# Kernel tuning notes

Measured on AMD Instinct MI355X. Metric: run time of the kernel, lower is better.

## Reference

```python
import jax, jax.numpy as jnp
import numpy as np

B, T, C, HS = 8, 2048, 1024, 64


def setup_inputs() -> dict:
    key = jax.random.key(0)
    kx, kq, kk, kv = jax.random.split(key, 4)
    x = jax.random.normal(kx, (B, T, C), dtype=jnp.float32)
    # torch Linear(C, HS, bias=False): weight [HS, C], y = x @ W.T -> store as [C, HS]
    Wq = jax.random.normal(kq, (C, HS), dtype=jnp.float32) * (C ** -0.5)
    Wk = jax.random.normal(kk, (C, HS), dtype=jnp.float32) * (C ** -0.5)
    Wv = jax.random.normal(kv, (C, HS), dtype=jnp.float32) * (C ** -0.5)
    return {"x": x, "Wq": Wq, "Wk": Wk, "Wv": Wv}


def reference(x, Wq, Wk, Wv):
    _, t, c = x.shape
    q = jnp.einsum('btc,ch->bth', x, Wq)
    k = jnp.einsum('btc,ch->bth', x, Wk)
    v = jnp.einsum('btc,ch->bth', x, Wv)
    # NOTE: original scales by C**-0.5 (hidden_dim), not head_size**-0.5
    scores = jnp.einsum('bth,bsh->bts', q, k) * (c ** -0.5)  # [B,T,T]
    causal = jnp.tril(jnp.ones((t, t), dtype=bool))
    scores = jnp.where(causal, scores, -jnp.inf)
    probs = jax.nn.softmax(scores, axis=-1)  # dropout p=0.0 -> identity
    out = jnp.einsum('bts,bsh->bth', probs, v)  # [B,T,HS]
    return out
```

## Files before the change

### kernel.cpp

```cpp
#include <hip/hip_runtime.h>
#include <hip/hip_bf16.h>

#define B_ 8
#define T_ 2048
#define C_ 1024
#define HS_ 64

typedef float f32x4 __attribute__((ext_vector_type(4)));
typedef __bf16 bf16x8 __attribute__((ext_vector_type(8)));
typedef __bf16 bf16x4 __attribute__((ext_vector_type(4)));


__global__ __launch_bounds__(256) void wt_kernel(const float* __restrict__ Wq,
                                                 const float* __restrict__ Wk,
                                                 const float* __restrict__ Wv,
                                                 __bf16* __restrict__ wt) {
    __shared__ float tile[64][65];
    int mb = blockIdx.x >> 4;
    int k0 = (blockIdx.x & 15) * 64;
    const float* W = (mb == 0) ? Wq : (mb == 1 ? Wk : Wv);
    int c = threadIdx.x & 63;
#pragma unroll
    for (int r = threadIdx.x >> 6; r < 64; r += 4)
        tile[r][c] = W[(size_t)(k0 + r) * 64 + c];
    __syncthreads();
    float scale = (mb == 0) ? 0.03125f : 1.0f;
    int kk = threadIdx.x & 63;
#pragma unroll
    for (int n = threadIdx.x >> 6; n < 64; n += 4)
        wt[(size_t)(mb * 64 + n) * C_ + k0 + kk] = (__bf16)(tile[kk][n] * scale);
}

__global__ __launch_bounds__(512) void qkv_kernel(const float* __restrict__ x,
                                                  const __bf16* __restrict__ wt,
                                                  __bf16* __restrict__ qf,
                                                  __bf16* __restrict__ kf,
                                                  __bf16* __restrict__ vf) {
    __shared__ __align__(16) char smem[57344];
    __bf16* xs0 = (__bf16*)smem;
    __bf16* xs1 = (__bf16*)(smem + 4096);
    __bf16* ws0 = (__bf16*)(smem + 8192);
    __bf16* ws1 = (__bf16*)(smem + 32768);

    const int tid = threadIdx.x;
    const int w = tid >> 6, lane = tid & 63, lq = lane & 15, lg = lane >> 4;
    const int m0 = blockIdx.x * 32;
    const int mt = w & 1;
    const int ntb = (w >> 1) * 3;

    f32x4 acc[3];
#pragma unroll
    for (int i = 0; i < 3; ++i) acc[i] = (f32x4)0.0f;

    const int xrow = tid >> 3, xch = tid & 7;
    float4 xr0, xr1;
    bf16x8 wr[3];

    if (tid < 256) {
        const float* xp = x + (size_t)(m0 + xrow) * C_ + xch * 8;
        xr0 = *(const float4*)xp;
        xr1 = *(const float4*)(xp + 4);
    }
#pragma unroll
    for (int s = 0; s < 3; ++s) {
        int u = tid + s * 512;
        wr[s] = *(const bf16x8*)(wt + (size_t)(u >> 3) * C_ + (u & 7) * 8);
    }
    if (tid < 256) {
        bf16x8 xb;
#pragma unroll
        for (int j = 0; j < 4; ++j) { xb[j] = (__bf16)xr0[j]; xb[4 + j] = (__bf16)xr1[j]; }
        *(bf16x8*)(xs0 + xrow * 64 + ((xch ^ (xrow & 7)) * 8)) = xb;
    }
#pragma unroll
    for (int s = 0; s < 3; ++s) {
        int u = tid + s * 512, rw = u >> 3, ch = u & 7;
        *(bf16x8*)(ws0 + rw * 64 + ((ch ^ (rw & 7)) * 8)) = wr[s];
    }

    for (int kt = 0; kt < 16; ++kt) {
        __syncthreads();
        __bf16* xsc = (kt & 1) ? xs1 : xs0;
        __bf16* wsc = (kt & 1) ? ws1 : ws0;
        if (kt < 15) {
            int k0 = (kt + 1) * 64;
            if (tid < 256) {
                const float* xp = x + (size_t)(m0 + xrow) * C_ + k0 + xch * 8;
                xr0 = *(const float4*)xp;
                xr1 = *(const float4*)(xp + 4);
            }
#pragma unroll
            for (int s = 0; s < 3; ++s) {
                int u = tid + s * 512;
                wr[s] = *(const bf16x8*)(wt + (size_t)(u >> 3) * C_ + k0 + (u & 7) * 8);
            }
        }
#pragma unroll
        for (int ks = 0; ks < 2; ++ks) {
            int r = mt * 16 + lq;
            bf16x8 a = *(const bf16x8*)(xsc + r * 64 + (((ks * 4 + lg) ^ (r & 7)) * 8));
#pragma unroll
            for (int i = 0; i < 3; ++i) {
                int rw = (ntb + i) * 16 + lq;
                bf16x8 b = *(const bf16x8*)(wsc + rw * 64 + (((ks * 4 + lg) ^ (rw & 7)) * 8));
                acc[i] = __builtin_amdgcn_mfma_f32_16x16x32_bf16(a, b, acc[i], 0, 0, 0);
            }
        }
        if (kt < 15) {
            __bf16* xsn = (kt & 1) ? xs0 : xs1;
            __bf16* wsn = (kt & 1) ? ws0 : ws1;
            if (tid < 256) {
                bf16x8 xb;
#pragma unroll
                for (int j = 0; j < 4; ++j) { xb[j] = (__bf16)xr0[j]; xb[4 + j] = (__bf16)xr1[j]; }
                *(bf16x8*)(xsn + xrow * 64 + ((xch ^ (xrow & 7)) * 8)) = xb;
            }
#pragma unroll
            for (int s = 0; s < 3; ++s) {
                int u = tid + s * 512, rw = u >> 3, ch = u & 7;
                *(bf16x8*)(wsn + rw * 64 + ((ch ^ (rw & 7)) * 8)) = wr[s];
            }
        }
    }
    __syncthreads();

    __bf16(*obuf)[208] = (__bf16(*)[208])smem;
#pragma unroll
    for (int i = 0; i < 3; ++i)
#pragma unroll
        for (int r = 0; r < 4; ++r)
            obuf[mt * 16 + lg * 4 + r][(ntb + i) * 16 + lq] = (__bf16)acc[i][r];
    __syncthreads();

    if (w < 4) {
        int mg = w & 1, half = w >> 1;
        size_t qt16 = (size_t)(m0 >> 4) + mg;
        bf16x8 vq = *(const bf16x8*)&obuf[mg * 16 + lq][half * 32 + lg * 8];
        bf16x8 vk = *(const bf16x8*)&obuf[mg * 16 + lq][64 + half * 32 + lg * 8];
        *(bf16x8*)(qf + ((qt16 * 2 + half) * 64 + lane) * 8) = vq;
        *(bf16x8*)(kf + ((qt16 * 2 + half) * 64 + lane) * 8) = vk;
    } else {
        int ntv = w - 4;
        bf16x8 vv;
#pragma unroll
        for (int j = 0; j < 8; ++j)
            vv[j] = obuf[lg * 8 + j][128 + ntv * 16 + lq];
        size_t kt32 = (size_t)(m0 >> 5);
        *(bf16x8*)(vf + ((kt32 * 4 + ntv) * 64 + lane) * 8) = vv;
    }
}

__global__ __launch_bounds__(512) void attn_kernel(const __bf16* __restrict__ qf,
                                                   const __bf16* __restrict__ kf,
                                                   const __bf16* __restrict__ vf,
                                                   float* __restrict__ out) {
    __shared__ float olds[8][16][64];
    __shared__ float mlds[8][16], llds[8][16];
    __shared__ __align__(16) __bf16 plds[8][16 * 40];

    int w    = threadIdx.x >> 6;
    int lane = threadIdx.x & 63;
    int lq = lane & 15, lg = lane >> 4;

    int b  = blockIdx.x & 7;
    int t0 = (blockIdx.x >> 3) * 16;

    size_t qbase = ((size_t)b * 128 + (t0 >> 4)) * 2;
    bf16x8 aq0 = *(const bf16x8*)(qf + ((qbase + 0) * 64 + lane) * 8);
    bf16x8 aq1 = *(const bf16x8*)(qf + ((qbase + 1) * 64 + lane) * 8);

    f32x4 o[4];
#pragma unroll
    for (int nt = 0; nt < 4; ++nt) o[nt] = (f32x4)0.0f;
    float m_s = -1e30f, l_s = 0.f;

    __bf16* pw = &plds[w][0];

    int ntiles = (t0 + 47) >> 5;
    for (int kt = w; kt < ntiles; kt += 8) {
        int s0 = kt * 32;
        f32x4 s[2];
#pragma unroll
        for (int ct = 0; ct < 2; ++ct) {
            size_t kbase = ((size_t)b * 128 + (s0 >> 4) + ct) * 2;
            bf16x8 k0 = *(const bf16x8*)(kf + ((kbase + 0) * 64 + lane) * 8);
            bf16x8 k1 = *(const bf16x8*)(kf + ((kbase + 1) * 64 + lane) * 8);
            f32x4 a = (f32x4)0.0f;
            a = __builtin_amdgcn_mfma_f32_16x16x32_bf16(k0, aq0, a, 0, 0, 0);
            a = __builtin_amdgcn_mfma_f32_16x16x32_bf16(k1, aq1, a, 0, 0, 0);
            s[ct] = a;
        }
        if (s0 + 31 > t0) {
#pragma unroll
            for (int ct = 0; ct < 2; ++ct)
#pragma unroll
                for (int r = 0; r < 4; ++r)
                    if (s0 + ct * 16 + lg * 4 + r > t0 + lq) s[ct][r] = -1e30f;
        }
        float pm = fmaxf(fmaxf(fmaxf(s[0][0], s[0][1]), fmaxf(s[0][2], s[0][3])),
                         fmaxf(fmaxf(s[1][0], s[1][1]), fmaxf(s[1][2], s[1][3])));
        pm = fmaxf(pm, __shfl_xor(pm, 16));
        pm = fmaxf(pm, __shfl_xor(pm, 32));
        float mn = fmaxf(m_s, pm);
        float al = __expf(m_s - mn);
        m_s = mn;
        f32x4 p0, p1;
#pragma unroll
        for (int r = 0; r < 4; ++r) {
            p0[r] = __expf(s[0][r] - mn);
            p1[r] = __expf(s[1][r] - mn);
        }
        float rs = (p0[0] + p0[1]) + (p0[2] + p0[3]) +
                   (p1[0] + p1[1]) + (p1[2] + p1[3]);
        rs += __shfl_xor(rs, 16);
        rs += __shfl_xor(rs, 32);
        l_s = l_s * al + rs;
        float alr[4];
#pragma unroll
        for (int r = 0; r < 4; ++r) alr[r] = __shfl(al, lg * 4 + r);
#pragma unroll
        for (int nt = 0; nt < 4; ++nt)
#pragma unroll
            for (int r = 0; r < 4; ++r) o[nt][r] *= alr[r];

        bf16x4 q0, q1;
#pragma unroll
        for (int r = 0; r < 4; ++r) { q0[r] = (__bf16)p0[r]; q1[r] = (__bf16)p1[r]; }
        *(bf16x4*)&pw[lq * 40 + lg * 4]      = q0;
        *(bf16x4*)&pw[lq * 40 + 16 + lg * 4] = q1;
        asm volatile("" ::: "memory");
        bf16x8 pa = *(const bf16x8*)&pw[lq * 40 + lg * 8];
#pragma unroll
        for (int nt = 0; nt < 4; ++nt) {
            bf16x8 bv = *(const bf16x8*)(vf +
                (((size_t)(b * 64 + (s0 >> 5)) * 4 + nt) * 64 + lane) * 8);
            o[nt] = __builtin_amdgcn_mfma_f32_16x16x32_bf16(pa, bv, o[nt], 0, 0, 0);
        }
    }

    asm volatile("" ::: "memory");
#pragma unroll
    for (int nt = 0; nt < 4; ++nt)
#pragma unroll
        for (int r = 0; r < 4; ++r)
            olds[w][lg * 4 + r][nt * 16 + lq] = o[nt][r];
    if (lg == 0) {
        mlds[w][lq] = m_s;
        llds[w][lq] = l_s;
    }
    __syncthreads();

    int row = threadIdx.x >> 5;
    int col = (threadIdx.x & 31) * 2;
    float M = -1e30f;
#pragma unroll
    for (int w2 = 0; w2 < 8; ++w2) M = fmaxf(M, mlds[w2][row]);
    float L = 0.f, o0 = 0.f, o1 = 0.f;
#pragma unroll
    for (int w2 = 0; w2 < 8; ++w2) {
        float sc = __expf(mlds[w2][row] - M);
        L  += sc * llds[w2][row];
        o0 += sc * olds[w2][row][col];
        o1 += sc * olds[w2][row][col + 1];
    }
    float inv = 1.0f / L;
    float* ob = out + ((size_t)b * T_ + t0 + row) * HS_ + col;
    ob[0] = o0 * inv;
    ob[1] = o1 * inv;
}

extern "C" void kernel_launch(void* const* d_in, const int* in_sizes, int n_in,
                              void* d_out, int out_size, void* d_ws, size_t ws_size,
                              hipStream_t stream) {
    const float* x  = (const float*)d_in[0];
    const float* Wq = (const float*)d_in[1];
    const float* Wk = (const float*)d_in[2];
    const float* Wv = (const float*)d_in[3];
    char* ws = (char*)d_ws;
    __bf16* wt = (__bf16*)ws;
    __bf16* qf = (__bf16*)(ws + 393216);
    __bf16* kf = (__bf16*)(ws + 2490368);
    __bf16* vf = (__bf16*)(ws + 4587520);
    float* out = (float*)d_out;

    wt_kernel<<<dim3(48), dim3(256), 0, stream>>>(Wq, Wk, Wv, wt);
    qkv_kernel<<<dim3(512), dim3(512), 0, stream>>>(x, wt, qf, kf, vf);
    attn_kernel<<<dim3(1024), dim3(512), 0, stream>>>(qf, kf, vf, out);
}
```

Measured before the change: 41.06 us.

## Split QKV projection across N halves and enlarge attention query tiles

The QKV projection now launches twice as many 256-thread blocks, each computing half of the 192 output columns, so more blocks are resident and LDS use drops. The attention kernel now handles 32 query rows per block with 4 waves over 64-key tiles, reuses each K/V load across two query subtiles, orders blocks heaviest-first, and adds setprio around the MFMA sections. The output merge is vectorized to float4. These changes aim at better load balance and fewer global K/V loads per unit of work, at the cost of more registers per wave and fewer waves per block to split the key range.

```diff
diff --git a/kernel.cpp b/kernel.cpp
--- a/kernel.cpp
+++ b/kernel.cpp
@@ -31,20 +31,22 @@
         wt[(size_t)(mb * 64 + n) * C_ + k0 + kk] = (__bf16)(tile[kk][n] * scale);
 }
 
-__global__ __launch_bounds__(512) void qkv_kernel(const float* __restrict__ x,
-                                                  const __bf16* __restrict__ wt,
-                                                  __bf16* __restrict__ qf,
-                                                  __bf16* __restrict__ kf,
-                                                  __bf16* __restrict__ vf) {
-    __shared__ __align__(16) char smem[57344];
+__global__ __launch_bounds__(256, 4) void qkv_kernel(const float* __restrict__ x,
+                                                     const __bf16* __restrict__ wt,
+                                                     __bf16* __restrict__ qf,
+                                                     __bf16* __restrict__ kf,
+                                                     __bf16* __restrict__ vf) {
+    __shared__ __align__(16) char smem[32768];
     __bf16* xs0 = (__bf16*)smem;
     __bf16* xs1 = (__bf16*)(smem + 4096);
     __bf16* ws0 = (__bf16*)(smem + 8192);
-    __bf16* ws1 = (__bf16*)(smem + 32768);
+    __bf16* ws1 = (__bf16*)(smem + 20480);
 
     const int tid = threadIdx.x;
     const int w = tid >> 6, lane = tid & 63, lq = lane & 15, lg = lane >> 4;
-    const int m0 = blockIdx.x * 32;
+    const int bid = blockIdx.x;
+    const int m0 = ((bid >> 4) * 8 + (bid & 7)) * 32;
+    const int n0 = ((bid >> 3) & 1) * 96;
     const int mt = w & 1;
     const int ntb = (w >> 1) * 3;
 
@@ -56,26 +58,24 @@
     float4 xr0, xr1;
     bf16x8 wr[3];
 
-    if (tid < 256) {
+    {
         const float* xp = x + (size_t)(m0 + xrow) * C_ + xch * 8;
         xr0 = *(const float4*)xp;
         xr1 = *(const float4*)(xp + 4);
-    }
-#pragma unroll
-    for (int s = 0; s < 3; ++s) {
-        int u = tid + s * 512;
-        wr[s] = *(const bf16x8*)(wt + (size_t)(u >> 3) * C_ + (u & 7) * 8);
-    }
-    if (tid < 256) {
+#pragma unroll
+        for (int s = 0; s < 3; ++s) {
+            int u = tid + s * 256;
+            wr[s] = *(const bf16x8*)(wt + (size_t)(n0 + (u >> 3)) * C_ + (u & 7) * 8);
+        }
         bf16x8 xb;
 #pragma unroll
         for (int j = 0; j < 4; ++j) { xb[j] = (__bf16)xr0[j]; xb[4 + j] = (__bf16)xr1[j]; }
         *(bf16x8*)(xs0 + xrow * 64 + ((xch ^ (xrow & 7)) * 8)) = xb;
-    }
-#pragma unroll
-    for (int s = 0; s < 3; ++s) {
-        int u = tid + s * 512, rw = u >> 3, ch = u & 7;
-        *(bf16x8*)(ws0 + rw * 64 + ((ch ^ (rw & 7)) * 8)) = wr[s];
+#pragma unroll
+        for (int s = 0; s < 3; ++s) {
+            int u = tid + s * 256, rw = u >> 3, ch = u & 7;
+            *(bf16x8*)(ws0 + rw * 64 + ((ch ^ (rw & 7)) * 8)) = wr[s];
+        }
     }
 
     for (int kt = 0; kt < 16; ++kt) {
@@ -84,15 +84,13 @@
         __bf16* wsc = (kt & 1) ? ws1 : ws0;
         if (kt < 15) {
             int k0 = (kt + 1) * 64;
-            if (tid < 256) {
-                const float* xp = x + (size_t)(m0 + xrow) * C_ + k0 + xch * 8;
-                xr0 = *(const float4*)xp;
-                xr1 = *(const float4*)(xp + 4);
-            }
+            const float* xp = x + (size_t)(m0 + xrow) * C_ + k0 + xch * 8;
+            xr0 = *(const float4*)xp;
+            xr1 = *(const float4*)(xp + 4);
 #pragma unroll
             for (int s = 0; s < 3; ++s) {
-                int u = tid + s * 512;
-                wr[s] = *(const bf16x8*)(wt + (size_t)(u >> 3) * C_ + k0 + (u & 7) * 8);
+                int u = tid + s * 256;
+                wr[s] = *(const bf16x8*)(wt + (size_t)(n0 + (u >> 3)) * C_ + k0 + (u & 7) * 8);
             }
         }
 #pragma unroll
@@ -109,22 +107,20 @@
         if (kt < 15) {
             __bf16* xsn = (kt & 1) ? xs0 : xs1;
             __bf16* wsn = (kt & 1) ? ws0 : ws1;
-            if (tid < 256) {
-                bf16x8 xb;
-#pragma unroll
-                for (int j = 0; j < 4; ++j) { xb[j] = (__bf16)xr0[j]; xb[4 + j] = (__bf16)xr1[j]; }
-                *(bf16x8*)(xsn + xrow * 64 + ((xch ^ (xrow & 7)) * 8)) = xb;
-            }
+            bf16x8 xb;
+#pragma unroll
+            for (int j = 0; j < 4; ++j) { xb[j] = (__bf16)xr0[j]; xb[4 + j] = (__bf16)xr1[j]; }
+            *(bf16x8*)(xsn + xrow * 64 + ((xch ^ (xrow & 7)) * 8)) = xb;
 #pragma unroll
             for (int s = 0; s < 3; ++s) {
-                int u = tid + s * 512, rw = u >> 3, ch = u & 7;
+                int u = tid + s * 256, rw = u >> 3, ch = u & 7;
                 *(bf16x8*)(wsn + rw * 64 + ((ch ^ (rw & 7)) * 8)) = wr[s];
             }
         }
     }
     __syncthreads();
 
-    __bf16(*obuf)[208] = (__bf16(*)[208])smem;
+    __bf16(*obuf)[104] = (__bf16(*)[104])smem;
 #pragma unroll
     for (int i = 0; i < 3; ++i)
 #pragma unroll
@@ -132,141 +128,191 @@
             obuf[mt * 16 + lg * 4 + r][(ntb + i) * 16 + lq] = (__bf16)acc[i][r];
     __syncthreads();
 
-    if (w < 4) {
-        int mg = w & 1, half = w >> 1;
+    if (n0 == 0) {
+        int mg = w & 1, hf = w >> 1;
         size_t qt16 = (size_t)(m0 >> 4) + mg;
-        bf16x8 vq = *(const bf16x8*)&obuf[mg * 16 + lq][half * 32 + lg * 8];
-        bf16x8 vk = *(const bf16x8*)&obuf[mg * 16 + lq][64 + half * 32 + lg * 8];
-        *(bf16x8*)(qf + ((qt16 * 2 + half) * 64 + lane) * 8) = vq;
-        *(bf16x8*)(kf + ((qt16 * 2 + half) * 64 + lane) * 8) = vk;
+        bf16x8 vq = *(const bf16x8*)&obuf[mg * 16 + lq][hf * 32 + lg * 8];
+        *(bf16x8*)(qf + ((qt16 * 2 + hf) * 64 + lane) * 8) = vq;
+        if (w < 2) {
+            bf16x8 vk = *(const bf16x8*)&obuf[w * 16 + lq][64 + lg * 8];
+            *(bf16x8*)(kf + (((size_t)(m0 >> 4) + w) * 2 * 64 + lane) * 8) = vk;
+        }
     } else {
-        int ntv = w - 4;
+        if (w < 2) {
+            bf16x8 vk = *(const bf16x8*)&obuf[w * 16 + lq][lg * 8];
+            *(bf16x8*)(kf + ((((size_t)(m0 >> 4) + w) * 2 + 1) * 64 + lane) * 8) = vk;
+        }
         bf16x8 vv;
 #pragma unroll
         for (int j = 0; j < 8; ++j)
-            vv[j] = obuf[lg * 8 + j][128 + ntv * 16 + lq];
+            vv[j] = obuf[lg * 8 + j][32 + w * 16 + lq];
         size_t kt32 = (size_t)(m0 >> 5);
-        *(bf16x8*)(vf + ((kt32 * 4 + ntv) * 64 + lane) * 8) = vv;
+        *(bf16x8*)(vf + ((kt32 * 4 + w) * 64 + lane) * 8) = vv;
     }
 }
 
-__global__ __launch_bounds__(512) void attn_kernel(const __bf16* __restrict__ qf,
-                                                   const __bf16* __restrict__ kf,
-                                                   const __bf16* __restrict__ vf,
-                                                   float* __restrict__ out) {
-    __shared__ float olds[8][16][64];
-    __shared__ float mlds[8][16], llds[8][16];
-    __shared__ __align__(16) __bf16 plds[8][16 * 40];
+__global__ __launch_bounds__(256, 3) void attn_kernel(const __bf16* __restrict__ qf,
+                                                      const __bf16* __restrict__ kf,
+                                                      const __bf16* __restrict__ vf,
+                                                      float* __restrict__ out) {
+    __shared__ __align__(16) char smem[4 * 4608];
+    __shared__ float mlds[4][16], llds[4][16];
 
     int w    = threadIdx.x >> 6;
     int lane = threadIdx.x & 63;
     int lq = lane & 15, lg = lane >> 4;
 
     int b  = blockIdx.x & 7;
-    int t0 = (blockIdx.x >> 3) * 16;
-
-    size_t qbase = ((size_t)b * 128 + (t0 >> 4)) * 2;
-    bf16x8 aq0 = *(const bf16x8*)(qf + ((qbase + 0) * 64 + lane) * 8);
-    bf16x8 aq1 = *(const bf16x8*)(qf + ((qbase + 1) * 64 + lane) * 8);
-
-    f32x4 o[4];
-#pragma unroll
-    for (int nt = 0; nt < 4; ++nt) o[nt] = (f32x4)0.0f;
-    float m_s = -1e30f, l_s = 0.f;
-
-    __bf16* pw = &plds[w][0];
-
-    int ntiles = (t0 + 47) >> 5;
-    for (int kt = w; kt < ntiles; kt += 8) {
-        int s0 = kt * 32;
-        f32x4 s[2];
-#pragma unroll
-        for (int ct = 0; ct < 2; ++ct) {
+    int q0 = (63 - (blockIdx.x >> 3)) * 32;
+
+    __bf16* pw = (__bf16*)(smem + w * 4608);
+
+    bf16x8 bq[2][2];
+#pragma unroll
+    for (int qs = 0; qs < 2; ++qs)
+#pragma unroll
+        for (int hf = 0; hf < 2; ++hf)
+            bq[qs][hf] = *(const bf16x8*)(qf +
+                ((((size_t)b * 128 + (q0 >> 4) + qs) * 2 + hf) * 64 + lane) * 8);
+
+    f32x4 o[2][4];
+#pragma unroll
+    for (int qs = 0; qs < 2; ++qs)
+#pragma unroll
+        for (int nt = 0; nt < 4; ++nt) o[qs][nt] = (f32x4)0.0f;
+    float m_s[2] = {-1e30f, -1e30f}, l_s[2] = {0.f, 0.f};
+
+    int ntiles = (q0 + 95) >> 6;
+    for (int kt = w; kt < ntiles; kt += 4) {
+        int s0 = kt * 64;
+        f32x4 s[2][4];
+        __builtin_amdgcn_s_setprio(1);
+#pragma unroll
+        for (int ct = 0; ct < 4; ++ct) {
             size_t kbase = ((size_t)b * 128 + (s0 >> 4) + ct) * 2;
             bf16x8 k0 = *(const bf16x8*)(kf + ((kbase + 0) * 64 + lane) * 8);
             bf16x8 k1 = *(const bf16x8*)(kf + ((kbase + 1) * 64 + lane) * 8);
-            f32x4 a = (f32x4)0.0f;
-            a = __builtin_amdgcn_mfma_f32_16x16x32_bf16(k0, aq0, a, 0, 0, 0);
-            a = __builtin_amdgcn_mfma_f32_16x16x32_bf16(k1, aq1, a, 0, 0, 0);
-            s[ct] = a;
-        }
-        if (s0 + 31 > t0) {
-#pragma unroll
-            for (int ct = 0; ct < 2; ++ct)
-#pragma unroll
-                for (int r = 0; r < 4; ++r)
-                    if (s0 + ct * 16 + lg * 4 + r > t0 + lq) s[ct][r] = -1e30f;
-        }
-        float pm = fmaxf(fmaxf(fmaxf(s[0][0], s[0][1]), fmaxf(s[0][2], s[0][3])),
-                         fmaxf(fmaxf(s[1][0], s[1][1]), fmaxf(s[1][2], s[1][3])));
-        pm = fmaxf(pm, __shfl_xor(pm, 16));
-        pm = fmaxf(pm, __shfl_xor(pm, 32));
-        float mn = fmaxf(m_s, pm);
-        float al = __expf(m_s - mn);
-        m_s = mn;
-        f32x4 p0, p1;
-#pragma unroll
-        for (int r = 0; r < 4; ++r) {
-            p0[r] = __expf(s[0][r] - mn);
-            p1[r] = __expf(s[1][r] - mn);
-        }
-        float rs = (p0[0] + p0[1]) + (p0[2] + p0[3]) +
-                   (p1[0] + p1[1]) + (p1[2] + p1[3]);
-        rs += __shfl_xor(rs, 16);
-        rs += __shfl_xor(rs, 32);
-        l_s = l_s * al + rs;
-        float alr[4];
-#pragma unroll
-        for (int r = 0; r < 4; ++r) alr[r] = __shfl(al, lg * 4 + r);
+#pragma unroll
+            for (int qs = 0; qs < 2; ++qs) {
+                f32x4 a = (f32x4)0.0f;
+                a = __builtin_amdgcn_mfma_f32_16x16x32_bf16(k0, bq[qs][0], a, 0, 0, 0);
+                a = __builtin_amdgcn_mfma_f32_16x16x32_bf16(k1, bq[qs][1], a, 0, 0, 0);
+                s[qs][ct] = a;
+            }
+        }
+        __builtin_amdgcn_s_setprio(0);
+        if (s0 + 63 > q0) {
+#pragma unroll
+            for (int qs = 0; qs < 2; ++qs)
+#pragma unroll
+                for (int ct = 0; ct < 4; ++ct)
+#pragma unroll
+                    for (int r = 0; r < 4; ++r)
+                        if (s0 + ct * 16 + lg * 4 + r > q0 + qs * 16 + lq)
+                            s[qs][ct][r] = -1e30f;
+        }
+        float al2[2];
+#pragma unroll
+        for (int qs = 0; qs < 2; ++qs) {
+            float pm = -1e30f;
+#pragma unroll
+            for (int ct = 0; ct < 4; ++ct)
+#pragma unroll
+                for (int r = 0; r < 4; ++r) pm = fmaxf(pm, s[qs][ct][r]);
+            pm = fmaxf(pm, __shfl_xor(pm, 16));
+            pm = fmaxf(pm, __shfl_xor(pm, 32));
+            float mn = fmaxf(m_s[qs], pm);
+            float al = __expf(m_s[qs] - mn);
+            m_s[qs] = mn;
+            float rs = 0.f;
+#pragma unroll
+            for (int ct = 0; ct < 4; ++ct)
+#pragma unroll
+                for (int r = 0; r < 4; ++r) {
+                    float p = __expf(s[qs][ct][r] - mn);
+                    s[qs][ct][r] = p;
+                    rs += p;
+                }
+            rs += __shfl_xor(rs, 16);
+            rs += __shfl_xor(rs, 32);
+            l_s[qs] = l_s[qs] * al + rs;
+            al2[qs] = al;
+        }
+#pragma unroll
+        for (int qs = 0; qs < 2; ++qs) {
+            float alr[4];
+#pragma unroll
+            for (int r = 0; r < 4; ++r) alr[r] = __shfl(al2[qs], lg * 4 + r);
+#pragma unroll
+            for (int nt = 0; nt < 4; ++nt)
+#pragma unroll
+                for (int r = 0; r < 4; ++r) o[qs][nt][r] *= alr[r];
+        }
+#pragma unroll
+        for (int qs = 0; qs < 2; ++qs)
+#pragma unroll
+            for (int ct = 0; ct < 4; ++ct) {
+                bf16x4 qv;
+#pragma unroll
+                for (int r = 0; r < 4; ++r) qv[r] = (__bf16)s[qs][ct][r];
+                *(bf16x4*)&pw[(qs * 16 + lq) * 72 + ct * 16 + lg * 4] = qv;
+            }
+        asm volatile("" ::: "memory");
+        bf16x8 bv[2][4];
+#pragma unroll
+        for (int ks = 0; ks < 2; ++ks)
+#pragma unroll
+            for (int nt = 0; nt < 4; ++nt)
+                bv[ks][nt] = *(const bf16x8*)(vf +
+                    (((size_t)(b * 64 + (s0 >> 5) + ks) * 4 + nt) * 64 + lane) * 8);
+        __builtin_amdgcn_s_setprio(1);
+#pragma unroll
+        for (int qs = 0; qs < 2; ++qs) {
+            bf16x8 pa0 = *(const bf16x8*)&pw[(qs * 16 + lq) * 72 + lg * 8];
+            bf16x8 pa1 = *(const bf16x8*)&pw[(qs * 16 + lq) * 72 + 32 + lg * 8];
+#pragma unroll
+            for (int nt = 0; nt < 4; ++nt) {
+                o[qs][nt] = __builtin_amdgcn_mfma_f32_16x16x32_bf16(pa0, bv[0][nt], o[qs][nt], 0, 0, 0);
+                o[qs][nt] = __builtin_amdgcn_mfma_f32_16x16x32_bf16(pa1, bv[1][nt], o[qs][nt], 0, 0, 0);
+            }
+        }
+        __builtin_amdgcn_s_setprio(0);
+    }
+
+    float* olds_w = (float*)(smem + w * 4608);
+#pragma unroll
+    for (int qs = 0; qs < 2; ++qs) {
+        __syncthreads();
 #pragma unroll
         for (int nt = 0; nt < 4; ++nt)
 #pragma unroll
-            for (int r = 0; r < 4; ++r) o[nt][r] *= alr[r];
-
-        bf16x4 q0, q1;
-#pragma unroll
-        for (int r = 0; r < 4; ++r) { q0[r] = (__bf16)p0[r]; q1[r] = (__bf16)p1[r]; }
-        *(bf16x4*)&pw[lq * 40 + lg * 4]      = q0;
-        *(bf16x4*)&pw[lq * 40 + 16 + lg * 4] = q1;
-        asm volatile("" ::: "memory");
-        bf16x8 pa = *(const bf16x8*)&pw[lq * 40 + lg * 8];
-#pragma unroll
-        for (int nt = 0; nt < 4; ++nt) {
-            bf16x8 bv = *(const bf16x8*)(vf +
-                (((size_t)(b * 64 + (s0 >> 5)) * 4 + nt) * 64 + lane) * 8);
-            o[nt] = __builtin_amdgcn_mfma_f32_16x16x32_bf16(pa, bv, o[nt], 0, 0, 0);
-        }
-    }
-
-    asm volatile("" ::: "memory");
-#pragma unroll
-    for (int nt = 0; nt < 4; ++nt)
-#pragma unroll
-        for (int r = 0; r < 4; ++r)
-            olds[w][lg * 4 + r][nt * 16 + lq] = o[nt][r];
-    if (lg == 0) {
-        mlds[w][lq] = m_s;
-        llds[w][lq] = l_s;
-    }
-    __syncthreads();
-
-    int row = threadIdx.x >> 5;
-    int col = (threadIdx.x & 31) * 2;
-    float M = -1e30f;
-#pragma unroll
-    for (int w2 = 0; w2 < 8; ++w2) M = fmaxf(M, mlds[w2][row]);
-    float L = 0.f, o0 = 0.f, o1 = 0.f;
-#pragma unroll
-    for (int w2 = 0; w2 < 8; ++w2) {
-        float sc = __expf(mlds[w2][row] - M);
-        L  += sc * llds[w2][row];
-        o0 += sc * olds[w2][row][col];
-        o1 += sc * olds[w2][row][col + 1];
-    }
-    float inv = 1.0f / L;
-    float* ob = out + ((size_t)b * T_ + t0 + row) * HS_ + col;
-    ob[0] = o0 * inv;
-    ob[1] = o1 * inv;
+            for (int r = 0; r < 4; ++r)
+                olds_w[(lg * 4 + r) * 64 + nt * 16 + lq] = o[qs][nt][r];
+        if (lg == 0) {
+            mlds[w][lq] = m_s[qs];
+            llds[w][lq] = l_s[qs];
+        }
+        __syncthreads();
+        int row = threadIdx.x >> 4;
+        int c4  = (threadIdx.x & 15) * 4;
+        float M = -1e30f;
+#pragma unroll
+        for (int w2 = 0; w2 < 4; ++w2) M = fmaxf(M, mlds[w2][row]);
+        float L = 0.f;
+        f32x4 oa = (f32x4)0.0f;
+#pragma unroll
+        for (int w2 = 0; w2 < 4; ++w2) {
+            float sc = __expf(mlds[w2][row] - M);
+            L += sc * llds[w2][row];
+            const float* op = (const float*)(smem + w2 * 4608) + row * 64 + c4;
+#pragma unroll
+            for (int j = 0; j < 4; ++j) oa[j] += sc * op[j];
+        }
+        float inv = 1.0f / L;
+        float4 st;
+        st.x = oa[0] * inv; st.y = oa[1] * inv; st.z = oa[2] * inv; st.w = oa[3] * inv;
+        *(float4*)(out + ((size_t)b * T_ + q0 + qs * 16 + row) * HS_ + c4) = st;
+    }
 }
 
 extern "C" void kernel_launch(void* const* d_in, const int* in_sizes, int n_in,
@@ -284,6 +330,6 @@
     float* out = (float*)d_out;
 
     wt_kernel<<<dim3(48), dim3(256), 0, stream>>>(Wq, Wk, Wv, wt);
-    qkv_kernel<<<dim3(512), dim3(512), 0, stream>>>(x, wt, qf, kf, vf);
-    attn_kernel<<<dim3(1024), dim3(512), 0, stream>>>(qf, kf, vf, out);
+    qkv_kernel<<<dim3(1024), dim3(256), 0, stream>>>(x, wt, qf, kf, vf);
+    attn_kernel<<<dim3(512), dim3(256), 0, stream>>>(qf, kf, vf, out);
 }
```

After: 53.43 us. 1.3x slower.
